# Kernel optimization log

Measured on AMD Instinct MI355X. Metric: run time of the kernel, lower is better.

Reference implementation:

```python
import jax, jax.numpy as jnp
import numpy as np

N = 50000          # nodes
E = 1600000        # edges (avg degree 32)
NUM_FEAT = 512
HIDDEN = 128
NUM_CLASS = 40
NUM_LAYERS = 4
EPS = 0.3


def setup_inputs() -> dict:
    key = jax.random.key(0)
    ks = jax.random.split(key, 8)
    x = jax.random.normal(ks[0], (N, NUM_FEAT), dtype=jnp.float32)
    edge_index = jax.random.randint(ks[1], (2, E), 0, N, dtype=jnp.int64)
    gain = 1.414  # xavier_normal_(gain=1.414) as in reset_parameters
    W1 = jax.random.normal(ks[2], (HIDDEN, NUM_FEAT), dtype=jnp.float32) * gain * (2.0 / (HIDDEN + NUM_FEAT)) ** 0.5
    b1 = jnp.zeros((HIDDEN,), dtype=jnp.float32)
    W2 = jax.random.normal(ks[3], (NUM_CLASS, HIDDEN), dtype=jnp.float32) * gain * (2.0 / (NUM_CLASS + HIDDEN)) ** 0.5
    b2 = jnp.zeros((NUM_CLASS,), dtype=jnp.float32)
    # FAConv attention vectors: Linear(channels, 1, bias=False) per layer
    att_l = jax.random.normal(ks[4], (NUM_LAYERS, HIDDEN), dtype=jnp.float32) * (2.0 / (1 + HIDDEN)) ** 0.5
    att_r = jax.random.normal(ks[5], (NUM_LAYERS, HIDDEN), dtype=jnp.float32) * (2.0 / (1 + HIDDEN)) ** 0.5
    return dict(x=x, edge_index=edge_index, W1=W1, b1=b1, W2=W2, b2=b2, att_l=att_l, att_r=att_r)


def reference(x, edge_index, W1, b1, W2, b2, att_l, att_r):
    n = x.shape[0]
    # gcn_norm with self-loops (FAConv default add_self_loops=True)
    loops = jnp.arange(n, dtype=edge_index.dtype)
    src = jnp.concatenate([edge_index[0], loops])  # source j
    dst = jnp.concatenate([edge_index[1], loops])  # target i
    deg = jax.ops.segment_sum(jnp.ones_like(src, dtype=x.dtype), dst, num_segments=n)
    dis = jax.lax.rsqrt(jnp.maximum(deg, 1.0))
    norm = dis[src] * dis[dst]  # [E+N]

    # eval mode: dropout is identity
    h = jax.nn.relu(x @ W1.T + b1)  # [N, HIDDEN]
    raw = h
    for l in range(NUM_LAYERS):
        al = h @ att_l[l]  # [N]
        ar = h @ att_r[l]  # [N]
        coef = jnp.tanh(al[src] + ar[dst]) * norm            # [E+N]
        agg = jax.ops.segment_sum(h[src] * coef[:, None], dst, num_segments=n)
        h = agg + EPS * raw
    logits = h @ W2.T + b2  # [N, NUM_CLASS]
    return jax.nn.log_softmax(logits, axis=1)
```

## Files before the change

### kernel.cpp

```cpp
#include <hip/hip_runtime.h>
#include <cmath>


#define HIDDEN 128
#define FEAT 512
#define NCLASS 40
#define LDST 40
#define LDSW 132
#define NB 256
#define PITCH 12544
#define BM1 64

typedef __attribute__((ext_vector_type(8))) short short8;
typedef __attribute__((ext_vector_type(4))) float f32x4;

__device__ __forceinline__ float bf_lo(unsigned u) { return __uint_as_float(u << 16); }
__device__ __forceinline__ float bf_hi(unsigned u) { return __uint_as_float(u & 0xffff0000u); }
__device__ __forceinline__ unsigned pack_bf16(float x, float y) {
    unsigned ux = __float_as_uint(x);
    unsigned uy = __float_as_uint(y);
    unsigned lx = (ux + 0x7fffu + ((ux >> 16) & 1u)) >> 16;
    unsigned hy = (uy + 0x7fffu + ((uy >> 16) & 1u)) & 0xffff0000u;
    return hy | lx;
}
__device__ __forceinline__ float fast_tanh(float x) {
    x = fminf(fmaxf(x, -15.f), 15.f);
    float e = __expf(2.f * x);
    return (e - 1.f) / (e + 1.f);
}

__global__ __launch_bounds__(256) void k_hist(const int* __restrict__ ei, int E, int CE,
                                              unsigned* __restrict__ partial,
                                              ushort* __restrict__ lrank) {
    __shared__ unsigned lh[PITCH];
    const int b = blockIdx.x, tid = threadIdx.x;
    for (int w = tid; w < PITCH; w += 256) lh[w] = 0;
    __syncthreads();
    int e0 = b * CE, e1 = min(E, e0 + CE);
    for (int e = e0 + tid; e < e1; e += 256) {
        int dst = ei[E + e];
        int sh = (dst & 3) * 8;
        unsigned old = atomicAdd(&lh[dst >> 2], 1u << sh);
        lrank[e] = (ushort)((old >> sh) & 0xffu);
    }
    __syncthreads();
    unsigned* prow = partial + (size_t)b * PITCH;
    for (int w = tid; w < PITCH; w += 256) prow[w] = lh[w];
}

__global__ void k_hscan(unsigned* __restrict__ partial, int* __restrict__ deg, int n) {
    int w = blockIdx.x * 256 + threadIdx.x;
    if (w >= PITCH) return;
    unsigned run = 0;
    size_t idx = w;
    for (int b = 0; b < NB; ++b, idx += PITCH) {
        unsigned v = partial[idx];
        partial[idx] = run;
        run += v;
    }
    int node = 4 * w;
    if (node < n)     deg[node]     = run & 0xffu;
    if (node + 1 < n) deg[node + 1] = (run >> 8) & 0xffu;
    if (node + 2 < n) deg[node + 2] = (run >> 16) & 0xffu;
    if (node + 3 < n) deg[node + 3] = run >> 24;
}

__global__ void k_dis(const int* __restrict__ deg, float* __restrict__ dis, int n) {
    int i = blockIdx.x * 256 + threadIdx.x;
    if (i < n) dis[i] = rsqrtf((float)(deg[i] + 1));
}

__global__ void k_scan1(const int* __restrict__ deg, int* __restrict__ offs,
                        int* __restrict__ part, int n) {
    __shared__ int s[256];
    int tid = threadIdx.x;
    int gid = blockIdx.x * 256 + tid;
    int v = (gid < n) ? deg[gid] : 0;
    s[tid] = v;
    __syncthreads();
    for (int off = 1; off < 256; off <<= 1) {
        int t = (tid >= off) ? s[tid - off] : 0;
        __syncthreads();
        s[tid] += t;
        __syncthreads();
    }
    if (gid < n) offs[gid] = s[tid] - v;
    if (tid == 255) part[blockIdx.x] = s[255];
}

__global__ void k_scan2(int* __restrict__ part, int nb) {
    __shared__ int s[256];
    int tid = threadIdx.x;
    int v = (tid < nb) ? part[tid] : 0;
    s[tid] = v;
    __syncthreads();
    for (int off = 1; off < 256; off <<= 1) {
        int t = (tid >= off) ? s[tid - off] : 0;
        __syncthreads();
        s[tid] += t;
        __syncthreads();
    }
    if (tid < nb) part[tid] = s[tid] - v;
}

__global__ void k_scan3(int* __restrict__ offs, const int* __restrict__ part, int n, int E) {
    int gid = blockIdx.x * 256 + threadIdx.x;
    if (gid < n) offs[gid] += part[blockIdx.x];
    if (gid == 0) offs[n] = E;
}

__global__ __launch_bounds__(256) void k_csr_fill(const int* __restrict__ ei, int E, int CE,
                                                  const int* __restrict__ offs,
                                                  const unsigned* __restrict__ partial,
                                                  const ushort* __restrict__ lrank,
                                                  int* __restrict__ csrc) {
    __shared__ unsigned lp[PITCH];
    const int b = blockIdx.x, tid = threadIdx.x;
    const unsigned* prow = partial + (size_t)b * PITCH;
    for (int w = tid; w < PITCH; w += 256) lp[w] = prow[w];
    __syncthreads();
    int e0 = b * CE, e1 = min(E, e0 + CE);
    for (int e = e0 + tid; e < e1; e += 256) {
        int dst = ei[E + e];
        int src = ei[e];
        unsigned wv = lp[dst >> 2];
        int base = (wv >> ((dst & 3) * 8)) & 0xffu;
        csrc[offs[dst] + base + (int)lrank[e]] = src;
    }
}

__global__ __launch_bounds__(256) void k_gemm1(const float* __restrict__ x,
                                               const float* __restrict__ W1,
                                               const float* __restrict__ b1,
                                               float* __restrict__ h, int M) {
    __shared__ ushort As[BM1 * LDST];
    __shared__ ushort Bs[128 * LDST];
    const int tid = threadIdx.x;
    const int bm = blockIdx.x * BM1;
    const int wave = tid >> 6, lane = tid & 63;
    const int rh = (wave >> 1) * 32;
    const int ch = (wave & 1) * 64;
    const int sub = lane & 15, quad = lane >> 4;
    const int lrow = tid >> 3;
    const int lcol = (tid & 7) * 4;
    f32x4 acc[2][4] = {};
    float4 av[2], bv[4];
#pragma unroll
    for (int i = 0; i < 2; ++i) {
        int grow = bm + lrow + 32 * i;
        av[i] = (grow < M) ? *(const float4*)(x + (size_t)grow * FEAT + lcol)
                           : make_float4(0.f, 0.f, 0.f, 0.f);
    }
#pragma unroll
    for (int i = 0; i < 4; ++i)
        bv[i] = *(const float4*)(W1 + (size_t)(lrow + 32 * i) * FEAT + lcol);

    for (int k0 = 0; k0 < FEAT; k0 += 32) {
#pragma unroll
        for (int i = 0; i < 2; ++i)
            *(uint2*)(As + (lrow + 32 * i) * LDST + lcol) =
                make_uint2(pack_bf16(av[i].x, av[i].y), pack_bf16(av[i].z, av[i].w));
#pragma unroll
        for (int i = 0; i < 4; ++i)
            *(uint2*)(Bs + (lrow + 32 * i) * LDST + lcol) =
                make_uint2(pack_bf16(bv[i].x, bv[i].y), pack_bf16(bv[i].z, bv[i].w));
        __syncthreads();
        if (k0 + 32 < FEAT) {
            const int kn = k0 + 32;
#pragma unroll
            for (int i = 0; i < 2; ++i) {
                int grow = bm + lrow + 32 * i;
                av[i] = (grow < M) ? *(const float4*)(x + (size_t)grow * FEAT + kn + lcol)
                                   : make_float4(0.f, 0.f, 0.f, 0.f);
            }
#pragma unroll
            for (int i = 0; i < 4; ++i)
                bv[i] = *(const float4*)(W1 + (size_t)(lrow + 32 * i) * FEAT + kn + lcol);
        }
        short8 af[2], bfr[4];
#pragma unroll
        for (int t = 0; t < 2; ++t)
            af[t] = *(const short8*)(As + (rh + t * 16 + sub) * LDST + quad * 8);
#pragma unroll
        for (int u = 0; u < 4; ++u)
            bfr[u] = *(const short8*)(Bs + (ch + u * 16 + sub) * LDST + quad * 8);
#pragma unroll
        for (int t = 0; t < 2; ++t)
#pragma unroll
            for (int u = 0; u < 4; ++u)
                acc[t][u] = __builtin_amdgcn_mfma_f32_16x16x32_bf16(af[t], bfr[u], acc[t][u], 0, 0, 0);
        __syncthreads();
    }
    float b1v[4];
#pragma unroll
    for (int u = 0; u < 4; ++u) b1v[u] = b1[ch + u * 16 + sub];
#pragma unroll
    for (int t = 0; t < 2; ++t) {
#pragma unroll
        for (int u = 0; u < 4; ++u) {
            int col = ch + u * 16 + sub;
#pragma unroll
            for (int r2 = 0; r2 < 4; ++r2) {
                int grow = bm + rh + t * 16 + quad * 4 + r2;
                if (grow < M)
                    h[(size_t)grow * HIDDEN + col] = fmaxf(acc[t][u][r2] + b1v[u], 0.f);
            }
        }
    }
}

__global__ void k_prep(const float* __restrict__ h, unsigned* __restrict__ hbf,
                       const float* __restrict__ attl, const float* __restrict__ attr,
                       const float* __restrict__ dis, float2* __restrict__ al2,
                       float* __restrict__ ar, int n) {
    int node = (blockIdx.x * blockDim.x + threadIdx.x) >> 6;
    int lane = threadIdx.x & 63;
    if (node >= n) return;
    float2 hv = ((const float2*)(h + (size_t)node * HIDDEN))[lane];
    hbf[(size_t)node * 64 + lane] = pack_bf16(hv.x, hv.y);
    float pl = hv.x * attl[2 * lane] + hv.y * attl[2 * lane + 1];
    float pr = hv.x * attr[2 * lane] + hv.y * attr[2 * lane + 1];
    for (int off = 32; off; off >>= 1) {
        pl += __shfl_down(pl, off);
        pr += __shfl_down(pr, off);
    }
    if (lane == 0) {
        al2[node] = make_float2(pl, dis[node]);
        ar[node] = pr;
    }
}

__global__ void k_coef(const float2* __restrict__ al2, const float* __restrict__ ar,
                       const int* __restrict__ offs, const int* __restrict__ csrc,
                       float* __restrict__ coef, float* __restrict__ selfc, int n) {
    int node = (blockIdx.x * blockDim.x + threadIdx.x) >> 6;
    int lane = threadIdx.x & 63;
    if (node >= n) return;
    const float2 self = al2[node];
    const float arn = ar[node];
    const float disn = self.y;
    if (lane == 0) selfc[node] = fast_tanh(self.x + arn) * disn * disn;
    int e0 = offs[node], e1 = offs[node + 1];
    for (int e = e0 + lane; e < e1; e += 64) {
        int s = csrc[e];
        float2 ls = al2[s];
        coef[e] = fast_tanh(ls.x + arn) * ls.y * disn;
    }
}

__global__ void k_aggregate(const unsigned* __restrict__ hbf, const float* __restrict__ raw,
                            const float* __restrict__ coef, const float* __restrict__ selfc,
                            const float* __restrict__ dis,
                            const int* __restrict__ offs, const int* __restrict__ csrc,
                            float* __restrict__ hout, unsigned* __restrict__ houtbf,
                            const float* __restrict__ attl_n, const float* __restrict__ attr_n,
                            float2* __restrict__ al2_o, float* __restrict__ ar_o, int n) {
    int node = (blockIdx.x * blockDim.x + threadIdx.x) >> 6;
    int lane = threadIdx.x & 63;
    if (node >= n) return;
    const int grp = lane >> 4;
    const int sub = lane & 15;
    float acc[8] = {0.f, 0.f, 0.f, 0.f, 0.f, 0.f, 0.f, 0.f};
    int e0 = offs[node], e1 = offs[node + 1];
    int e = e0;
    for (; e + 16 <= e1; e += 16) {
        int sa = csrc[e + grp];
        int sb = csrc[e + 4 + grp];
        int sc = csrc[e + 8 + grp];
        int sd = csrc[e + 12 + grp];
        float ca = coef[e + grp];
        float cb = coef[e + 4 + grp];
        float cc = coef[e + 8 + grp];
        float cd = coef[e + 12 + grp];
        uint4 ra = *(const uint4*)(hbf + (size_t)sa * 64 + sub * 4);
        uint4 rb = *(const uint4*)(hbf + (size_t)sb * 64 + sub * 4);
        uint4 rc = *(const uint4*)(hbf + (size_t)sc * 64 + sub * 4);
        uint4 rd = *(const uint4*)(hbf + (size_t)sd * 64 + sub * 4);
        acc[0] += ca * bf_lo(ra.x); acc[1] += ca * bf_hi(ra.x);
        acc[2] += ca * bf_lo(ra.y); acc[3] += ca * bf_hi(ra.y);
        acc[4] += ca * bf_lo(ra.z); acc[5] += ca * bf_hi(ra.z);
        acc[6] += ca * bf_lo(ra.w); acc[7] += ca * bf_hi(ra.w);
        acc[0] += cb * bf_lo(rb.x); acc[1] += cb * bf_hi(rb.x);
        acc[2] += cb * bf_lo(rb.y); acc[3] += cb * bf_hi(rb.y);
        acc[4] += cb * bf_lo(rb.z); acc[5] += cb * bf_hi(rb.z);
        acc[6] += cb * bf_lo(rb.w); acc[7] += cb * bf_hi(rb.w);
        acc[0] += cc * bf_lo(rc.x); acc[1] += cc * bf_hi(rc.x);
        acc[2] += cc * bf_lo(rc.y); acc[3] += cc * bf_hi(rc.y);
        acc[4] += cc * bf_lo(rc.z); acc[5] += cc * bf_hi(rc.z);
        acc[6] += cc * bf_lo(rc.w); acc[7] += cc * bf_hi(rc.w);
        acc[0] += cd * bf_lo(rd.x); acc[1] += cd * bf_hi(rd.x);
        acc[2] += cd * bf_lo(rd.y); acc[3] += cd * bf_hi(rd.y);
        acc[4] += cd * bf_lo(rd.z); acc[5] += cd * bf_hi(rd.z);
        acc[6] += cd * bf_lo(rd.w); acc[7] += cd * bf_hi(rd.w);
    }
    for (; e + 4 <= e1; e += 4) {
        int sa = csrc[e + grp];
        float ca = coef[e + grp];
        uint4 ra = *(const uint4*)(hbf + (size_t)sa * 64 + sub * 4);
        acc[0] += ca * bf_lo(ra.x); acc[1] += ca * bf_hi(ra.x);
        acc[2] += ca * bf_lo(ra.y); acc[3] += ca * bf_hi(ra.y);
        acc[4] += ca * bf_lo(ra.z); acc[5] += ca * bf_hi(ra.z);
        acc[6] += ca * bf_lo(ra.w); acc[7] += ca * bf_hi(ra.w);
    }
#pragma unroll
    for (int j = 0; j < 8; ++j) {
        acc[j] += __shfl_xor(acc[j], 16);
        acc[j] += __shfl_xor(acc[j], 32);
    }
    for (; e < e1; ++e) {
        int s = csrc[e];
        float c = coef[e];
        uint4 r = *(const uint4*)(hbf + (size_t)s * 64 + sub * 4);
        acc[0] += c * bf_lo(r.x); acc[1] += c * bf_hi(r.x);
        acc[2] += c * bf_lo(r.y); acc[3] += c * bf_hi(r.y);
        acc[4] += c * bf_lo(r.z); acc[5] += c * bf_hi(r.z);
        acc[6] += c * bf_lo(r.w); acc[7] += c * bf_hi(r.w);
    }
    {
        float c = selfc[node];
        uint4 r = *(const uint4*)(hbf + (size_t)node * 64 + sub * 4);
        acc[0] += c * bf_lo(r.x); acc[1] += c * bf_hi(r.x);
        acc[2] += c * bf_lo(r.y); acc[3] += c * bf_hi(r.y);
        acc[4] += c * bf_lo(r.z); acc[5] += c * bf_hi(r.z);
        acc[6] += c * bf_lo(r.w); acc[7] += c * bf_hi(r.w);
    }
    float o[8];
    {
        float4 rv0 = *(const float4*)(raw + (size_t)node * HIDDEN + sub * 8);
        float4 rv1 = *(const float4*)(raw + (size_t)node * HIDDEN + sub * 8 + 4);
        o[0] = acc[0] + 0.3f * rv0.x; o[1] = acc[1] + 0.3f * rv0.y;
        o[2] = acc[2] + 0.3f * rv0.z; o[3] = acc[3] + 0.3f * rv0.w;
        o[4] = acc[4] + 0.3f * rv1.x; o[5] = acc[5] + 0.3f * rv1.y;
        o[6] = acc[6] + 0.3f * rv1.z; o[7] = acc[7] + 0.3f * rv1.w;
    }
    const float disn = dis[node];
    if (grp == 0) {
        *(float4*)(hout + (size_t)node * HIDDEN + sub * 8) = make_float4(o[0], o[1], o[2], o[3]);
        *(float4*)(hout + (size_t)node * HIDDEN + sub * 8 + 4) = make_float4(o[4], o[5], o[6], o[7]);
        if (houtbf) {
            uint4 pk = make_uint4(pack_bf16(o[0], o[1]), pack_bf16(o[2], o[3]),
                                  pack_bf16(o[4], o[5]), pack_bf16(o[6], o[7]));
            *(uint4*)(houtbf + (size_t)node * 64 + sub * 4) = pk;
        }
    }
    if (attl_n) {
        float4 a0 = *(const float4*)(attl_n + sub * 8);
        float4 a1 = *(const float4*)(attl_n + sub * 8 + 4);
        float4 c0 = *(const float4*)(attr_n + sub * 8);
        float4 c1 = *(const float4*)(attr_n + sub * 8 + 4);
        float pl = o[0] * a0.x + o[1] * a0.y + o[2] * a0.z + o[3] * a0.w +
                   o[4] * a1.x + o[5] * a1.y + o[6] * a1.z + o[7] * a1.w;
        float pr = o[0] * c0.x + o[1] * c0.y + o[2] * c0.z + o[3] * c0.w +
                   o[4] * c1.x + o[5] * c1.y + o[6] * c1.z + o[7] * c1.w;
        for (int off = 8; off; off >>= 1) {
            pl += __shfl_xor(pl, off);
            pr += __shfl_xor(pr, off);
        }
        if (lane == 0) {
            al2_o[node] = make_float2(pl, disn);
            ar_o[node] = pr;
        }
    }
}

__global__ __launch_bounds__(256, 4) void k_out(const float* __restrict__ h,
                                                const float* __restrict__ W2,
                                                const float* __restrict__ b2,
                                                float* __restrict__ out, int n) {
    __shared__ float ws[NCLASS * LDSW];
    __shared__ float bs[NCLASS];
    const int tid = threadIdx.x;
    for (int i = tid; i < NCLASS * (HIDDEN / 4); i += 256) {
        int r = i >> 5;
        int c4 = i & 31;
        *(float4*)(ws + r * LDSW + c4 * 4) = ((const float4*)W2)[i];
    }
    if (tid < NCLASS) bs[tid] = b2[tid];
    __syncthreads();
    int node = blockIdx.x * 32 + (tid >> 3);
    const int ol = tid & 7;
    if (node >= n) return;
    const float* hr = h + (size_t)node * HIDDEN;
    float acc[5];
#pragma unroll
    for (int c = 0; c < 5; ++c) acc[c] = bs[ol + 8 * c];
#pragma unroll
    for (int k0 = 0; k0 < HIDDEN; k0 += 16) {
        float4 h0 = *(const float4*)(hr + k0);
        float4 h1 = *(const float4*)(hr + k0 + 4);
        float4 h2v = *(const float4*)(hr + k0 + 8);
        float4 h3 = *(const float4*)(hr + k0 + 12);
#pragma unroll
        for (int c = 0; c < 5; ++c) {
            const float* w = ws + (ol + 8 * c) * LDSW + k0;
            float4 w0 = *(const float4*)(w);
            float4 w1 = *(const float4*)(w + 4);
            float4 w2v = *(const float4*)(w + 8);
            float4 w3 = *(const float4*)(w + 12);
            acc[c] += h0.x * w0.x + h0.y * w0.y + h0.z * w0.z + h0.w * w0.w +
                      h1.x * w1.x + h1.y * w1.y + h1.z * w1.z + h1.w * w1.w +
                      h2v.x * w2v.x + h2v.y * w2v.y + h2v.z * w2v.z + h2v.w * w2v.w +
                      h3.x * w3.x + h3.y * w3.y + h3.z * w3.z + h3.w * w3.w;
        }
    }
    float m = acc[0];
#pragma unroll
    for (int c = 1; c < 5; ++c) m = fmaxf(m, acc[c]);
    m = fmaxf(m, __shfl_xor(m, 1));
    m = fmaxf(m, __shfl_xor(m, 2));
    m = fmaxf(m, __shfl_xor(m, 4));
    float ssum = 0.f;
#pragma unroll
    for (int c = 0; c < 5; ++c) ssum += expf(acc[c] - m);
    ssum += __shfl_xor(ssum, 1);
    ssum += __shfl_xor(ssum, 2);
    ssum += __shfl_xor(ssum, 4);
    float lse = m + logf(ssum);
    float* orow = out + (size_t)node * NCLASS;
#pragma unroll
    for (int c = 0; c < 5; ++c) orow[ol + 8 * c] = acc[c] - lse;
}

extern "C" void kernel_launch(void* const* d_in, const int* in_sizes, int n_in,
                              void* d_out, int out_size, void* d_ws, size_t ws_size,
                              hipStream_t stream) {
    const float* x    = (const float*)d_in[0];
    const int*   ei   = (const int*)d_in[1];
    const float* W1   = (const float*)d_in[2];
    const float* b1   = (const float*)d_in[3];
    const float* W2   = (const float*)d_in[4];
    const float* b2   = (const float*)d_in[5];
    const float* attl = (const float*)d_in[6];
    const float* attr = (const float*)d_in[7];
    const int N = in_sizes[0] / FEAT;
    const int E = in_sizes[1] / 2;
    float* out = (float*)d_out;

    char* p = (char*)d_ws;
    auto take = [&](size_t bytes) {
        void* q = (void*)p;
        p += (bytes + 255) & ~(size_t)255;
        return q;
    };
    float*    h0   = (float*)take((size_t)N * HIDDEN * 4);
    float*    h1   = (float*)take((size_t)N * HIDDEN * 4);
    float*    h2   = (float*)take((size_t)N * HIDDEN * 4);
    unsigned* hb0  = (unsigned*)take((size_t)N * 64 * 4);
    unsigned* hb1  = (unsigned*)take((size_t)N * 64 * 4);
    int*      deg  = (int*)take((size_t)N * 4);
    float*    dis  = (float*)take((size_t)N * 4);
    int*      offs = (int*)take((size_t)(N + 1) * 4);
    unsigned* partial = (unsigned*)take((size_t)NB * PITCH * 4);
    ushort*   lrank   = (ushort*)take((size_t)E * 2);
    int*      csrc = (int*)take((size_t)E * 4);
    float2*   al2A = (float2*)take((size_t)N * 8);
    float2*   al2B = (float2*)take((size_t)N * 8);
    float*    arA  = (float*)take((size_t)N * 4);
    float*    arB  = (float*)take((size_t)N * 4);
    int*      part = (int*)take(1024);

    float*    coef  = (float*)partial;
    float*    selfc = coef + E;

    const int nbl = (N + 255) / 256;
    const int CE = (E + NB - 1) / NB;

    k_hist<<<NB, 256, 0, stream>>>(ei, E, CE, partial, lrank);
    k_hscan<<<(PITCH + 255) / 256, 256, 0, stream>>>(partial, deg, N);
    k_dis<<<nbl, 256, 0, stream>>>(deg, dis, N);
    k_scan1<<<nbl, 256, 0, stream>>>(deg, offs, part, N);
    k_scan2<<<1, 256, 0, stream>>>(part, nbl);
    k_scan3<<<nbl, 256, 0, stream>>>(offs, part, N, E);
    k_csr_fill<<<NB, 256, 0, stream>>>(ei, E, CE, offs, partial, lrank, csrc);

    k_gemm1<<<(N + BM1 - 1) / BM1, 256, 0, stream>>>(x, W1, b1, h0, N);
    k_prep<<<(N + 3) / 4, 256, 0, stream>>>(h0, hb0, attl, attr, dis, al2A, arA, N);

    float*    fout[4] = {h1, h2, h1, h2};
    unsigned* hbin = hb0, *hbout = hb1;
    float2*   alin = al2A, *alout = al2B;
    float*    arin = arA,  *arout = arB;
    for (int l = 0; l < 4; ++l) {
        const float* attl_n = (l < 3) ? (attl + (l + 1) * HIDDEN) : nullptr;
        const float* attr_n = (l < 3) ? (attr + (l + 1) * HIDDEN) : nullptr;
        unsigned* hbo = (l < 3) ? hbout : nullptr;
        k_coef<<<(N + 3) / 4, 256, 0, stream>>>(alin, arin, offs, csrc, coef, selfc, N);
        k_aggregate<<<(N + 3) / 4, 256, 0, stream>>>(hbin, h0, coef, selfc, dis, offs, csrc,
                                                     fout[l], hbo, attl_n, attr_n,
                                                     alout, arout, N);
        unsigned* tb = hbin; hbin = hbout; hbout = tb;
        float2* ta = alin; alin = alout; alout = ta;
        float* tr = arin; arin = arout; arout = tr;
    }

    k_out<<<(N + 31) / 32, 256, 0, stream>>>(h2, W2, b2, out, N);
}
```

Baseline: 584.0 us.

## Fuse edge coefficient computation into aggregation via wave shuffles

Removes the separate k_coef pass: each wave now loads up to 64 neighbor indices, computes the tanh attention coefficients in registers, and broadcasts index and coefficient with shuffles during the gather. This avoids writing and re-reading the per-edge coef array and one launch per layer. It also folds the k_dis kernel into k_hscan and adds launch bounds to several kernels. The tail handling now covers counts that are not a multiple of 4 by using zero coefficients, with self-index padding for out-of-range lanes.

```diff
diff --git a/kernel.cpp b/kernel.cpp
--- a/kernel.cpp
+++ b/kernel.cpp
@@ -48,7 +48,9 @@
     for (int w = tid; w < PITCH; w += 256) prow[w] = lh[w];
 }
 
-__global__ void k_hscan(unsigned* __restrict__ partial, int* __restrict__ deg, int n) {
+__global__ __launch_bounds__(256) void k_hscan(unsigned* __restrict__ partial,
+                                               int* __restrict__ deg,
+                                               float* __restrict__ dis, int n) {
     int w = blockIdx.x * 256 + threadIdx.x;
     if (w >= PITCH) return;
     unsigned run = 0;
@@ -59,19 +61,15 @@
         run += v;
     }
     int node = 4 * w;
-    if (node < n)     deg[node]     = run & 0xffu;
-    if (node + 1 < n) deg[node + 1] = (run >> 8) & 0xffu;
-    if (node + 2 < n) deg[node + 2] = (run >> 16) & 0xffu;
-    if (node + 3 < n) deg[node + 3] = run >> 24;
-}
-
-__global__ void k_dis(const int* __restrict__ deg, float* __restrict__ dis, int n) {
-    int i = blockIdx.x * 256 + threadIdx.x;
-    if (i < n) dis[i] = rsqrtf((float)(deg[i] + 1));
-}
-
-__global__ void k_scan1(const int* __restrict__ deg, int* __restrict__ offs,
-                        int* __restrict__ part, int n) {
+    int d0 = run & 0xffu, d1 = (run >> 8) & 0xffu, d2 = (run >> 16) & 0xffu, d3 = run >> 24;
+    if (node < n)     { deg[node]     = d0; dis[node]     = rsqrtf((float)(d0 + 1)); }
+    if (node + 1 < n) { deg[node + 1] = d1; dis[node + 1] = rsqrtf((float)(d1 + 1)); }
+    if (node + 2 < n) { deg[node + 2] = d2; dis[node + 2] = rsqrtf((float)(d2 + 1)); }
+    if (node + 3 < n) { deg[node + 3] = d3; dis[node + 3] = rsqrtf((float)(d3 + 1)); }
+}
+
+__global__ __launch_bounds__(256) void k_scan1(const int* __restrict__ deg, int* __restrict__ offs,
+                                               int* __restrict__ part, int n) {
     __shared__ int s[256];
     int tid = threadIdx.x;
     int gid = blockIdx.x * 256 + tid;
@@ -88,7 +86,7 @@
     if (tid == 255) part[blockIdx.x] = s[255];
 }
 
-__global__ void k_scan2(int* __restrict__ part, int nb) {
+__global__ __launch_bounds__(256) void k_scan2(int* __restrict__ part, int nb) {
     __shared__ int s[256];
     int tid = threadIdx.x;
     int v = (tid < nb) ? part[tid] : 0;
@@ -103,7 +101,8 @@
     if (tid < nb) part[tid] = s[tid] - v;
 }
 
-__global__ void k_scan3(int* __restrict__ offs, const int* __restrict__ part, int n, int E) {
+__global__ __launch_bounds__(256) void k_scan3(int* __restrict__ offs, const int* __restrict__ part,
+                                               int n, int E) {
     int gid = blockIdx.x * 256 + threadIdx.x;
     if (gid < n) offs[gid] += part[blockIdx.x];
     if (gid == 0) offs[n] = E;
@@ -209,7 +208,7 @@
     }
 }
 
-__global__ void k_prep(const float* __restrict__ h, unsigned* __restrict__ hbf,
+__global__ __launch_bounds__(256) void k_prep(const float* __restrict__ h, unsigned* __restrict__ hbf,
                        const float* __restrict__ attl, const float* __restrict__ attr,
                        const float* __restrict__ dis, float2* __restrict__ al2,
                        float* __restrict__ ar, int n) {
@@ -230,27 +229,9 @@
     }
 }
 
-__global__ void k_coef(const float2* __restrict__ al2, const float* __restrict__ ar,
-                       const int* __restrict__ offs, const int* __restrict__ csrc,
-                       float* __restrict__ coef, float* __restrict__ selfc, int n) {
-    int node = (blockIdx.x * blockDim.x + threadIdx.x) >> 6;
-    int lane = threadIdx.x & 63;
-    if (node >= n) return;
-    const float2 self = al2[node];
-    const float arn = ar[node];
-    const float disn = self.y;
-    if (lane == 0) selfc[node] = fast_tanh(self.x + arn) * disn * disn;
-    int e0 = offs[node], e1 = offs[node + 1];
-    for (int e = e0 + lane; e < e1; e += 64) {
-        int s = csrc[e];
-        float2 ls = al2[s];
-        coef[e] = fast_tanh(ls.x + arn) * ls.y * disn;
-    }
-}
-
-__global__ void k_aggregate(const unsigned* __restrict__ hbf, const float* __restrict__ raw,
-                            const float* __restrict__ coef, const float* __restrict__ selfc,
-                            const float* __restrict__ dis,
+__global__ __launch_bounds__(256) void k_aggregate(
+                            const unsigned* __restrict__ hbf, const float* __restrict__ raw,
+                            const float2* __restrict__ al2, const float* __restrict__ ar,
                             const int* __restrict__ offs, const int* __restrict__ csrc,
                             float* __restrict__ hout, unsigned* __restrict__ houtbf,
                             const float* __restrict__ attl_n, const float* __restrict__ attr_n,
@@ -260,64 +241,65 @@
     if (node >= n) return;
     const int grp = lane >> 4;
     const int sub = lane & 15;
+    const float arn = ar[node];
+    const float2 selfld = al2[node];
+    const float disn = selfld.y;
     float acc[8] = {0.f, 0.f, 0.f, 0.f, 0.f, 0.f, 0.f, 0.f};
     int e0 = offs[node], e1 = offs[node + 1];
-    int e = e0;
-    for (; e + 16 <= e1; e += 16) {
-        int sa = csrc[e + grp];
-        int sb = csrc[e + 4 + grp];
-        int sc = csrc[e + 8 + grp];
-        int sd = csrc[e + 12 + grp];
-        float ca = coef[e + grp];
-        float cb = coef[e + 4 + grp];
-        float cc = coef[e + 8 + grp];
-        float cd = coef[e + 12 + grp];
-        uint4 ra = *(const uint4*)(hbf + (size_t)sa * 64 + sub * 4);
-        uint4 rb = *(const uint4*)(hbf + (size_t)sb * 64 + sub * 4);
-        uint4 rc = *(const uint4*)(hbf + (size_t)sc * 64 + sub * 4);
-        uint4 rd = *(const uint4*)(hbf + (size_t)sd * 64 + sub * 4);
-        acc[0] += ca * bf_lo(ra.x); acc[1] += ca * bf_hi(ra.x);
-        acc[2] += ca * bf_lo(ra.y); acc[3] += ca * bf_hi(ra.y);
-        acc[4] += ca * bf_lo(ra.z); acc[5] += ca * bf_hi(ra.z);
-        acc[6] += ca * bf_lo(ra.w); acc[7] += ca * bf_hi(ra.w);
-        acc[0] += cb * bf_lo(rb.x); acc[1] += cb * bf_hi(rb.x);
-        acc[2] += cb * bf_lo(rb.y); acc[3] += cb * bf_hi(rb.y);
-        acc[4] += cb * bf_lo(rb.z); acc[5] += cb * bf_hi(rb.z);
-        acc[6] += cb * bf_lo(rb.w); acc[7] += cb * bf_hi(rb.w);
-        acc[0] += cc * bf_lo(rc.x); acc[1] += cc * bf_hi(rc.x);
-        acc[2] += cc * bf_lo(rc.y); acc[3] += cc * bf_hi(rc.y);
-        acc[4] += cc * bf_lo(rc.z); acc[5] += cc * bf_hi(rc.z);
-        acc[6] += cc * bf_lo(rc.w); acc[7] += cc * bf_hi(rc.w);
-        acc[0] += cd * bf_lo(rd.x); acc[1] += cd * bf_hi(rd.x);
-        acc[2] += cd * bf_lo(rd.y); acc[3] += cd * bf_hi(rd.y);
-        acc[4] += cd * bf_lo(rd.z); acc[5] += cd * bf_hi(rd.z);
-        acc[6] += cd * bf_lo(rd.w); acc[7] += cd * bf_hi(rd.w);
-    }
-    for (; e + 4 <= e1; e += 4) {
-        int sa = csrc[e + grp];
-        float ca = coef[e + grp];
-        uint4 ra = *(const uint4*)(hbf + (size_t)sa * 64 + sub * 4);
-        acc[0] += ca * bf_lo(ra.x); acc[1] += ca * bf_hi(ra.x);
-        acc[2] += ca * bf_lo(ra.y); acc[3] += ca * bf_hi(ra.y);
-        acc[4] += ca * bf_lo(ra.z); acc[5] += ca * bf_hi(ra.z);
-        acc[6] += ca * bf_lo(ra.w); acc[7] += ca * bf_hi(ra.w);
+    for (int base = e0; base < e1; base += 64) {
+        int cnt = min(64, e1 - base);
+        int idx = base + lane;
+        int smy = (lane < cnt) ? csrc[idx] : node;
+        float2 lmy = al2[smy];
+        float cmy = (lane < cnt) ? fast_tanh(lmy.x + arn) * lmy.y * disn : 0.f;
+        int t = 0;
+        for (; t + 16 <= cnt; t += 16) {
+            int sa = __shfl(smy, t + grp);
+            int sb = __shfl(smy, t + 4 + grp);
+            int sc = __shfl(smy, t + 8 + grp);
+            int sd = __shfl(smy, t + 12 + grp);
+            float ca = __shfl(cmy, t + grp);
+            float cb = __shfl(cmy, t + 4 + grp);
+            float cc = __shfl(cmy, t + 8 + grp);
+            float cd = __shfl(cmy, t + 12 + grp);
+            uint4 ra = *(const uint4*)(hbf + (size_t)sa * 64 + sub * 4);
+            uint4 rb = *(const uint4*)(hbf + (size_t)sb * 64 + sub * 4);
+            uint4 rc = *(const uint4*)(hbf + (size_t)sc * 64 + sub * 4);
+            uint4 rd = *(const uint4*)(hbf + (size_t)sd * 64 + sub * 4);
+            acc[0] += ca * bf_lo(ra.x); acc[1] += ca * bf_hi(ra.x);
+            acc[2] += ca * bf_lo(ra.y); acc[3] += ca * bf_hi(ra.y);
+            acc[4] += ca * bf_lo(ra.z); acc[5] += ca * bf_hi(ra.z);
+            acc[6] += ca * bf_lo(ra.w); acc[7] += ca * bf_hi(ra.w);
+            acc[0] += cb * bf_lo(rb.x); acc[1] += cb * bf_hi(rb.x);
+            acc[2] += cb * bf_lo(rb.y); acc[3] += cb * bf_hi(rb.y);
+            acc[4] += cb * bf_lo(rb.z); acc[5] += cb * bf_hi(rb.z);
+            acc[6] += cb * bf_lo(rb.w); acc[7] += cb * bf_hi(rb.w);
+            acc[0] += cc * bf_lo(rc.x); acc[1] += cc * bf_hi(rc.x);
+            acc[2] += cc * bf_lo(rc.y); acc[3] += cc * bf_hi(rc.y);
+            acc[4] += cc * bf_lo(rc.z); acc[5] += cc * bf_hi(rc.z);
+            acc[6] += cc * bf_lo(rc.w); acc[7] += cc * bf_hi(rc.w);
+            acc[0] += cd * bf_lo(rd.x); acc[1] += cd * bf_hi(rd.x);
+            acc[2] += cd * bf_lo(rd.y); acc[3] += cd * bf_hi(rd.y);
+            acc[4] += cd * bf_lo(rd.z); acc[5] += cd * bf_hi(rd.z);
+            acc[6] += cd * bf_lo(rd.w); acc[7] += cd * bf_hi(rd.w);
+        }
+        for (; t < cnt; t += 4) {
+            int sa = __shfl(smy, t + grp);
+            float ca = __shfl(cmy, t + grp);
+            uint4 ra = *(const uint4*)(hbf + (size_t)sa * 64 + sub * 4);
+            acc[0] += ca * bf_lo(ra.x); acc[1] += ca * bf_hi(ra.x);
+            acc[2] += ca * bf_lo(ra.y); acc[3] += ca * bf_hi(ra.y);
+            acc[4] += ca * bf_lo(ra.z); acc[5] += ca * bf_hi(ra.z);
+            acc[6] += ca * bf_lo(ra.w); acc[7] += ca * bf_hi(ra.w);
+        }
     }
 #pragma unroll
     for (int j = 0; j < 8; ++j) {
         acc[j] += __shfl_xor(acc[j], 16);
         acc[j] += __shfl_xor(acc[j], 32);
     }
-    for (; e < e1; ++e) {
-        int s = csrc[e];
-        float c = coef[e];
-        uint4 r = *(const uint4*)(hbf + (size_t)s * 64 + sub * 4);
-        acc[0] += c * bf_lo(r.x); acc[1] += c * bf_hi(r.x);
-        acc[2] += c * bf_lo(r.y); acc[3] += c * bf_hi(r.y);
-        acc[4] += c * bf_lo(r.z); acc[5] += c * bf_hi(r.z);
-        acc[6] += c * bf_lo(r.w); acc[7] += c * bf_hi(r.w);
-    }
     {
-        float c = selfc[node];
+        float c = fast_tanh(selfld.x + arn) * disn * disn;
         uint4 r = *(const uint4*)(hbf + (size_t)node * 64 + sub * 4);
         acc[0] += c * bf_lo(r.x); acc[1] += c * bf_hi(r.x);
         acc[2] += c * bf_lo(r.y); acc[3] += c * bf_hi(r.y);
@@ -333,7 +315,6 @@
         o[4] = acc[4] + 0.3f * rv1.x; o[5] = acc[5] + 0.3f * rv1.y;
         o[6] = acc[6] + 0.3f * rv1.z; o[7] = acc[7] + 0.3f * rv1.w;
     }
-    const float disn = dis[node];
     if (grp == 0) {
         *(float4*)(hout + (size_t)node * HIDDEN + sub * 8) = make_float4(o[0], o[1], o[2], o[3]);
         *(float4*)(hout + (size_t)node * HIDDEN + sub * 8 + 4) = make_float4(o[4], o[5], o[6], o[7]);
@@ -459,15 +440,11 @@
     float*    arB  = (float*)take((size_t)N * 4);
     int*      part = (int*)take(1024);
 
-    float*    coef  = (float*)partial;
-    float*    selfc = coef + E;
-
     const int nbl = (N + 255) / 256;
     const int CE = (E + NB - 1) / NB;
 
     k_hist<<<NB, 256, 0, stream>>>(ei, E, CE, partial, lrank);
-    k_hscan<<<(PITCH + 255) / 256, 256, 0, stream>>>(partial, deg, N);
-    k_dis<<<nbl, 256, 0, stream>>>(deg, dis, N);
+    k_hscan<<<(PITCH + 255) / 256, 256, 0, stream>>>(partial, deg, dis, N);
     k_scan1<<<nbl, 256, 0, stream>>>(deg, offs, part, N);
     k_scan2<<<1, 256, 0, stream>>>(part, nbl);
     k_scan3<<<nbl, 256, 0, stream>>>(offs, part, N, E);
@@ -484,8 +461,7 @@
         const float* attl_n = (l < 3) ? (attl + (l + 1) * HIDDEN) : nullptr;
         const float* attr_n = (l < 3) ? (attr + (l + 1) * HIDDEN) : nullptr;
         unsigned* hbo = (l < 3) ? hbout : nullptr;
-        k_coef<<<(N + 3) / 4, 256, 0, stream>>>(alin, arin, offs, csrc, coef, selfc, N);
-        k_aggregate<<<(N + 3) / 4, 256, 0, stream>>>(hbin, h0, coef, selfc, dis, offs, csrc,
+        k_aggregate<<<(N + 3) / 4, 256, 0, stream>>>(hbin, h0, alin, arin, offs, csrc,
                                                      fout[l], hbo, attl_n, attr_n,
                                                      alout, arout, N);
         unsigned* tb = hbin; hbin = hbout; hbout = tb;
```

Result: faster. 523.0 us (-10.5%).
